# Kernel tuning notes

Measured on AMD Instinct MI355X. Metric: run time of the kernel, lower is better.

## Reference

```python
import jax, jax.numpy as jnp
import numpy as np

N = 200_000          # total nodes
C = 256              # in_channels
B = 64               # batch_size (num graphs)
NPG = N // B         # nodes per graph = max_num_nodes = 3125
E = 3_200_000        # edges (avg degree 16)
RATIO = 0.5
MULTIPLIER = 1.0


def setup_inputs() -> dict:
    key = jax.random.key(0)
    k1, k2, k3, k4, k5, k6 = jax.random.split(key, 6)
    x = jax.random.normal(k1, (N, C), dtype=jnp.float32)
    # hk.initializers.TruncatedNormal() ~ truncated normal, stddev 1
    p = jax.random.truncated_normal(k2, -2.0, 2.0, (C,), dtype=jnp.float32)
    # edges constrained within each graph (realistic graph batching)
    g = jax.random.randint(k3, (E,), 0, B, dtype=jnp.int32)
    senders = g * NPG + jax.random.randint(k4, (E,), 0, NPG, dtype=jnp.int32)
    receivers = g * NPG + jax.random.randint(k5, (E,), 0, NPG, dtype=jnp.int32)
    # sorted batch vector: graph id per node
    batch = jnp.arange(N, dtype=jnp.int32) // NPG
    return {"x": x, "p": p, "senders": senders, "receivers": receivers, "batch": batch}


def _segment_softmax(score, batch, num_segments):
    # batch_softmax from haiku-geometric: numerically-stable per-graph softmax
    mx = jax.ops.segment_max(score, batch, num_segments=num_segments)
    e = jnp.exp(score - mx[batch])
    denom = jax.ops.segment_sum(e, batch, num_segments=num_segments)
    return e / denom[batch]


def reference(x, p, senders, receivers, batch):
    batch_size = B
    num_nodes = x.shape[0]
    # per-node score: <x_i, p>, then softmax within each graph
    score = jnp.sum(x * p, axis=-1)                       # [N]
    score = _segment_softmax(score, batch, batch_size)    # [N]

    # select_batch_topk: keep first k nodes (by position) per graph,
    # move the rest to a new batch id == batch_size.
    nodes_per_batch = jax.ops.segment_sum(
        jnp.ones(num_nodes, dtype=jnp.int32), batch, num_segments=batch_size)
    cum_num_nodes = jnp.concatenate(
        [jnp.zeros(1, jnp.int32), jnp.cumsum(nodes_per_batch)[:-1].astype(jnp.int32)])
    # ratio < 1 branch
    k = jnp.ceil(RATIO * nodes_per_batch).astype(jnp.int32)   # [B]
    index_batch = jnp.arange(num_nodes, dtype=jnp.int32) - cum_num_nodes[batch]
    threshold_per_batch = k[batch] - 1
    new_batch = jnp.where(index_batch <= threshold_per_batch,
                          batch, jnp.full(batch.shape, batch_size, dtype=batch.dtype))

    # gate features by score (multiplier == 1 -> no extra scale)
    x_gated = x * score[:, None]

    # stable sort nodes so dropped nodes go to the end
    new_perm = jnp.argsort(new_batch)          # stable
    x_out = x_gated[new_perm]
    new_batch_sorted = new_batch[new_perm]

    # turn edges touching dropped nodes into self-loops (faithful to source,
    # including the sequential where-overwrite of senders then receivers)
    new_batch_idx = jnp.max(batch) + 1
    mask = (new_batch_sorted[senders] == new_batch_idx) | \
           (new_batch_sorted[receivers] == new_batch_idx)
    senders_out = jnp.where(mask, receivers, senders)
    receivers_out = jnp.where(mask, senders_out, receivers)
    return x_out, senders_out, receivers_out, new_batch_sorted
```

## Files before the change

kernel.cpp:

```cpp
#include <hip/hip_runtime.h>
#include <hip/hip_bf16.h>
#include <stdint.h>


#define RATIO 0.5f

typedef float f32x4 __attribute__((ext_vector_type(4)));
typedef int   i32x4 __attribute__((ext_vector_type(4)));

__global__ __launch_bounds__(256) void k1_scores_boundary(
    const float* __restrict__ x, const float* __restrict__ p,
    const int* __restrict__ batch,
    float* __restrict__ s, int* __restrict__ start, int N) {
    int node0 = blockIdx.x * 8 + (threadIdx.x >> 6) * 2;
    int lane = threadIdx.x & 63;
    if (node0 >= N) return;
    int node1 = node0 + 1;
    const f32x4 pv = *reinterpret_cast<const f32x4*>(p + lane * 4);
    const f32x4 a = *reinterpret_cast<const f32x4*>(x + (size_t)node0 * 256 + lane * 4);
    const f32x4 b = *reinterpret_cast<const f32x4*>(x + (size_t)node1 * 256 + lane * 4);
    float acc0 = a.x * pv.x + a.y * pv.y + a.z * pv.z + a.w * pv.w;
    float acc1 = b.x * pv.x + b.y * pv.y + b.z * pv.z + b.w * pv.w;
    #pragma unroll
    for (int off = 32; off; off >>= 1) {
        acc0 += __shfl_down(acc0, off, 64);
        acc1 += __shfl_down(acc1, off, 64);
    }
    if (lane == 0) {
        s[node0] = acc0;
        s[node1] = acc1;
        int b0 = batch[node0];
        if (node0 == 0 || batch[node0 - 1] != b0) start[b0] = node0;
        int b1 = batch[node1];
        if (batch[node0] != b1) start[b1] = node1;
    }
}

__global__ __launch_bounds__(256) void k2_meta_stats(
    const float* __restrict__ s, const int* __restrict__ start, int N, int B,
    int* __restrict__ kk, int* __restrict__ Kb, int* __restrict__ Db,
    int* __restrict__ Ktot, float* __restrict__ mx, float* __restrict__ denom) {
    if (blockIdx.x == (unsigned)B) {
        int g = threadIdx.x;
        if (g >= B) return;
        int st = start[g];
        int en = (g == B - 1) ? N : start[g + 1];
        int cnt = en - st;
        int kv = (int)ceilf(RATIO * (float)cnt);
        int dv = cnt - kv;
        int kp = kv, dp = dv;
        #pragma unroll
        for (int off = 1; off < 64; off <<= 1) {
            int a = __shfl_up(kp, off, 64);
            int b_ = __shfl_up(dp, off, 64);
            if (g >= off) { kp += a; dp += b_; }
        }
        kk[g] = kv;
        Kb[g] = kp - kv;
        Db[g] = dp - dv;
        if (g == B - 1) *Ktot = kp;
        return;
    }
    int g = blockIdx.x;
    int st = start[g];
    int en = (g == B - 1) ? N : start[g + 1];
    __shared__ float red[256];
    float m = -INFINITY;
    for (int i = st + threadIdx.x; i < en; i += 256) m = fmaxf(m, s[i]);
    red[threadIdx.x] = m; __syncthreads();
    for (int o = 128; o; o >>= 1) {
        if (threadIdx.x < o) red[threadIdx.x] = fmaxf(red[threadIdx.x], red[threadIdx.x + o]);
        __syncthreads();
    }
    m = red[0]; __syncthreads();
    float sum = 0.f;
    for (int i = st + threadIdx.x; i < en; i += 256) sum += expf(s[i] - m);
    red[threadIdx.x] = sum; __syncthreads();
    for (int o = 128; o; o >>= 1) {
        if (threadIdx.x < o) red[threadIdx.x] += red[threadIdx.x + o];
        __syncthreads();
    }
    if (threadIdx.x == 0) { mx[g] = m; denom[g] = red[0]; }
}

__global__ __launch_bounds__(256) void k3_scatter(
    const float* __restrict__ x, const float* __restrict__ s,
    const int* __restrict__ batch, const int* __restrict__ start,
    const int* __restrict__ kk, const int* __restrict__ Kb, const int* __restrict__ Db,
    const int* __restrict__ Ktot, const float* __restrict__ mx, const float* __restrict__ denom,
    int N, int B, float* __restrict__ xout, float* __restrict__ nbout) {
    int node0 = blockIdx.x * 8 + (threadIdx.x >> 6) * 2;
    if (node0 >= N) return;
    int node1 = node0 + 1;
    int lane = threadIdx.x & 63;
    int kt = *Ktot;

    int g0 = batch[node0], g1 = batch[node1];
    int idx0 = node0 - start[g0], idx1 = node1 - start[g1];
    int kv0 = kk[g0], kv1 = kk[g1];
    bool kept0 = idx0 < kv0, kept1 = idx1 < kv1;
    int pos0 = kept0 ? (Kb[g0] + idx0) : (kt + Db[g0] + (idx0 - kv0));
    int pos1 = kept1 ? (Kb[g1] + idx1) : (kt + Db[g1] + (idx1 - kv1));
    float sc0 = expf(s[node0] - mx[g0]) / denom[g0];
    float sc1 = expf(s[node1] - mx[g1]) / denom[g1];

    const f32x4 a = *reinterpret_cast<const f32x4*>(x + (size_t)node0 * 256 + lane * 4);
    const f32x4 b = *reinterpret_cast<const f32x4*>(x + (size_t)node1 * 256 + lane * 4);
    f32x4 oa, ob;
    oa.x = a.x * sc0; oa.y = a.y * sc0; oa.z = a.z * sc0; oa.w = a.w * sc0;
    ob.x = b.x * sc1; ob.y = b.y * sc1; ob.z = b.z * sc1; ob.w = b.w * sc1;
    __builtin_nontemporal_store(oa, reinterpret_cast<f32x4*>(xout + (size_t)pos0 * 256 + lane * 4));
    __builtin_nontemporal_store(ob, reinterpret_cast<f32x4*>(xout + (size_t)pos1 * 256 + lane * 4));
    if (lane == 0) {
        __builtin_nontemporal_store((float)(kept0 ? g0 : B), nbout + pos0);
        __builtin_nontemporal_store((float)(kept1 ? g1 : B), nbout + pos1);
    }
}

__global__ __launch_bounds__(256) void k4_edges(
    const int* __restrict__ snd, const int* __restrict__ rcv, int E,
    const int* __restrict__ Ktot,
    float* __restrict__ sout, float* __restrict__ rout) {
    int t = blockIdx.x * blockDim.x + threadIdx.x;
    long base = (long)t * 8;
    if (base >= E) return;
    int kt = *Ktot;
    if (base + 8 <= E) {
        i32x4 s0 = __builtin_nontemporal_load(reinterpret_cast<const i32x4*>(snd + base));
        i32x4 s1 = __builtin_nontemporal_load(reinterpret_cast<const i32x4*>(snd + base + 4));
        i32x4 r0 = __builtin_nontemporal_load(reinterpret_cast<const i32x4*>(rcv + base));
        i32x4 r1 = __builtin_nontemporal_load(reinterpret_cast<const i32x4*>(rcv + base + 4));
        f32x4 so0, so1, ro0, ro1;
        so0.x = (float)(((s0.x >= kt) || (r0.x >= kt)) ? r0.x : s0.x);
        so0.y = (float)(((s0.y >= kt) || (r0.y >= kt)) ? r0.y : s0.y);
        so0.z = (float)(((s0.z >= kt) || (r0.z >= kt)) ? r0.z : s0.z);
        so0.w = (float)(((s0.w >= kt) || (r0.w >= kt)) ? r0.w : s0.w);
        so1.x = (float)(((s1.x >= kt) || (r1.x >= kt)) ? r1.x : s1.x);
        so1.y = (float)(((s1.y >= kt) || (r1.y >= kt)) ? r1.y : s1.y);
        so1.z = (float)(((s1.z >= kt) || (r1.z >= kt)) ? r1.z : s1.z);
        so1.w = (float)(((s1.w >= kt) || (r1.w >= kt)) ? r1.w : s1.w);
        ro0.x = (float)r0.x; ro0.y = (float)r0.y; ro0.z = (float)r0.z; ro0.w = (float)r0.w;
        ro1.x = (float)r1.x; ro1.y = (float)r1.y; ro1.z = (float)r1.z; ro1.w = (float)r1.w;
        __builtin_nontemporal_store(so0, reinterpret_cast<f32x4*>(sout + base));
        __builtin_nontemporal_store(so1, reinterpret_cast<f32x4*>(sout + base + 4));
        __builtin_nontemporal_store(ro0, reinterpret_cast<f32x4*>(rout + base));
        __builtin_nontemporal_store(ro1, reinterpret_cast<f32x4*>(rout + base + 4));
    } else {
        for (long e = base; e < E; ++e) {
            int sv = snd[e], rv = rcv[e];
            bool m = (sv >= kt) || (rv >= kt);
            sout[e] = (float)(m ? rv : sv);
            rout[e] = (float)rv;
        }
    }
}

extern "C" void kernel_launch(void* const* d_in, const int* in_sizes, int n_in,
                              void* d_out, int out_size, void* d_ws, size_t ws_size,
                              hipStream_t stream) {
    const float* x = (const float*)d_in[0];
    const float* p = (const float*)d_in[1];
    const int* senders = (const int*)d_in[2];
    const int* receivers = (const int*)d_in[3];
    const int* batch = (const int*)d_in[4];

    const int C = in_sizes[1];
    const int E = in_sizes[2];
    const int N = in_sizes[4];
    const int B = 64;

    char* ws = (char*)d_ws;
    float* s   = (float*)ws;
    int* start = (int*)(ws + (size_t)N * 4);
    int* kk    = start + B;
    int* Kb    = kk + B;
    int* Db    = Kb + B;
    int* Ktot  = Db + B;
    float* mx    = (float*)(Ktot + 1);
    float* denom = mx + B;

    float* out   = (float*)d_out;
    float* xout  = out;
    float* sout  = out + (size_t)N * C;
    float* rout  = sout + E;
    float* nbout = rout + E;

    k1_scores_boundary<<<(N + 7) / 8, 256, 0, stream>>>(x, p, batch, s, start, N);
    k2_meta_stats     <<<B + 1, 256, 0, stream>>>(s, start, N, B, kk, Kb, Db, Ktot, mx, denom);
    k3_scatter        <<<(N + 7) / 8, 256, 0, stream>>>(x, s, batch, start, kk, Kb, Db, Ktot,
                                                        mx, denom, N, B, xout, nbout);
    k4_edges          <<<((E + 7) / 8 + 255) / 256, 256, 0, stream>>>(senders, receivers, E,
                                                                      Ktot, sout, rout);
}
```

Measured before the change: 114.8 us.

## Fuse four kernels into one cooperative persistent kernel with grid syncs

```diff
diff --git a/kernel.cpp b/kernel.cpp
--- a/kernel.cpp
+++ b/kernel.cpp
@@ -1,6 +1,9 @@
 #include <hip/hip_runtime.h>
 #include <hip/hip_bf16.h>
+#include <hip/hip_cooperative_groups.h>
 #include <stdint.h>
+
+namespace cg = cooperative_groups;
 
 
 #define RATIO 0.5f
@@ -8,41 +11,70 @@
 typedef float f32x4 __attribute__((ext_vector_type(4)));
 typedef int   i32x4 __attribute__((ext_vector_type(4)));
 
-__global__ __launch_bounds__(256) void k1_scores_boundary(
+__global__ __launch_bounds__(256) void mega(
     const float* __restrict__ x, const float* __restrict__ p,
+    const int* __restrict__ snd, const int* __restrict__ rcv,
     const int* __restrict__ batch,
-    float* __restrict__ s, int* __restrict__ start, int N) {
-    int node0 = blockIdx.x * 8 + (threadIdx.x >> 6) * 2;
-    int lane = threadIdx.x & 63;
-    if (node0 >= N) return;
-    int node1 = node0 + 1;
-    const f32x4 pv = *reinterpret_cast<const f32x4*>(p + lane * 4);
-    const f32x4 a = *reinterpret_cast<const f32x4*>(x + (size_t)node0 * 256 + lane * 4);
-    const f32x4 b = *reinterpret_cast<const f32x4*>(x + (size_t)node1 * 256 + lane * 4);
-    float acc0 = a.x * pv.x + a.y * pv.y + a.z * pv.z + a.w * pv.w;
-    float acc1 = b.x * pv.x + b.y * pv.y + b.z * pv.z + b.w * pv.w;
-    #pragma unroll
-    for (int off = 32; off; off >>= 1) {
-        acc0 += __shfl_down(acc0, off, 64);
-        acc1 += __shfl_down(acc1, off, 64);
+    float* __restrict__ s, int* __restrict__ start,
+    int* __restrict__ kk, int* __restrict__ Kb, int* __restrict__ Db,
+    int* __restrict__ Ktot, float* __restrict__ mx, float* __restrict__ denom,
+    float* __restrict__ xout, float* __restrict__ nbout,
+    float* __restrict__ sout, float* __restrict__ rout,
+    int N, int B, int E) {
+    cg::grid_group grid = cg::this_grid();
+    const int lane = threadIdx.x & 63;
+    const int wid = blockIdx.x * (blockDim.x >> 6) + (threadIdx.x >> 6);
+    const int nwaves = gridDim.x * (blockDim.x >> 6);
+    const int npairs = N >> 1;
+
+    {
+        const f32x4 pv = *reinterpret_cast<const f32x4*>(p + lane * 4);
+        for (int pr = wid; pr < npairs; pr += nwaves) {
+            int node0 = pr * 2, node1 = node0 + 1;
+            const f32x4 a = *reinterpret_cast<const f32x4*>(x + (size_t)node0 * 256 + lane * 4);
+            const f32x4 b = *reinterpret_cast<const f32x4*>(x + (size_t)node1 * 256 + lane * 4);
+            float acc0 = a.x * pv.x + a.y * pv.y + a.z * pv.z + a.w * pv.w;
+            float acc1 = b.x * pv.x + b.y * pv.y + b.z * pv.z + b.w * pv.w;
+            #pragma unroll
+            for (int off = 32; off; off >>= 1) {
+                acc0 += __shfl_down(acc0, off, 64);
+                acc1 += __shfl_down(acc1, off, 64);
+            }
+            if (lane == 0) {
+                s[node0] = acc0;
+                s[node1] = acc1;
+                int b0 = batch[node0];
+                if (node0 == 0 || batch[node0 - 1] != b0) start[b0] = node0;
+                int b1 = batch[node1];
+                if (b0 != b1) start[b1] = node1;
+            }
+        }
     }
-    if (lane == 0) {
-        s[node0] = acc0;
-        s[node1] = acc1;
-        int b0 = batch[node0];
-        if (node0 == 0 || batch[node0 - 1] != b0) start[b0] = node0;
-        int b1 = batch[node1];
-        if (batch[node0] != b1) start[b1] = node1;
-    }
-}
+    grid.sync();
 
-__global__ __launch_bounds__(256) void k2_meta_stats(
-    const float* __restrict__ s, const int* __restrict__ start, int N, int B,
-    int* __restrict__ kk, int* __restrict__ Kb, int* __restrict__ Db,
-    int* __restrict__ Ktot, float* __restrict__ mx, float* __restrict__ denom) {
-    if (blockIdx.x == (unsigned)B) {
+    if (blockIdx.x < (unsigned)B) {
+        int g = blockIdx.x;
+        int st = start[g];
+        int en = (g == B - 1) ? N : start[g + 1];
+        __shared__ float red[256];
+        float m = -INFINITY;
+        for (int i = st + threadIdx.x; i < en; i += 256) m = fmaxf(m, s[i]);
+        red[threadIdx.x] = m; __syncthreads();
+        for (int o = 128; o; o >>= 1) {
+            if (threadIdx.x < o) red[threadIdx.x] = fmaxf(red[threadIdx.x], red[threadIdx.x + o]);
+            __syncthreads();
+        }
+        m = red[0]; __syncthreads();
+        float sum = 0.f;
+        for (int i = st + threadIdx.x; i < en; i += 256) sum += expf(s[i] - m);
+        red[threadIdx.x] = sum; __syncthreads();
+        for (int o = 128; o; o >>= 1) {
+            if (threadIdx.x < o) red[threadIdx.x] += red[threadIdx.x + o];
+            __syncthreads();
+        }
+        if (threadIdx.x == 0) { mx[g] = m; denom[g] = red[0]; }
+    } else if (blockIdx.x == (unsigned)B && threadIdx.x < 64) {
         int g = threadIdx.x;
-        if (g >= B) return;
         int st = start[g];
         int en = (g == B - 1) ? N : start[g + 1];
         int cnt = en - st;
@@ -59,98 +91,66 @@
         Kb[g] = kp - kv;
         Db[g] = dp - dv;
         if (g == B - 1) *Ktot = kp;
-        return;
     }
-    int g = blockIdx.x;
-    int st = start[g];
-    int en = (g == B - 1) ? N : start[g + 1];
-    __shared__ float red[256];
-    float m = -INFINITY;
-    for (int i = st + threadIdx.x; i < en; i += 256) m = fmaxf(m, s[i]);
-    red[threadIdx.x] = m; __syncthreads();
-    for (int o = 128; o; o >>= 1) {
-        if (threadIdx.x < o) red[threadIdx.x] = fmaxf(red[threadIdx.x], red[threadIdx.x + o]);
-        __syncthreads();
+    grid.sync();
+
+    const int kt = *Ktot;
+    for (int pr = wid; pr < npairs; pr += nwaves) {
+        int node0 = pr * 2, node1 = node0 + 1;
+        int g0 = batch[node0], g1 = batch[node1];
+        int idx0 = node0 - start[g0], idx1 = node1 - start[g1];
+        int kv0 = kk[g0], kv1 = kk[g1];
+        bool kept0 = idx0 < kv0, kept1 = idx1 < kv1;
+        int pos0 = kept0 ? (Kb[g0] + idx0) : (kt + Db[g0] + (idx0 - kv0));
+        int pos1 = kept1 ? (Kb[g1] + idx1) : (kt + Db[g1] + (idx1 - kv1));
+        float sc0 = expf(s[node0] - mx[g0]) / denom[g0];
+        float sc1 = expf(s[node1] - mx[g1]) / denom[g1];
+        const f32x4 a = *reinterpret_cast<const f32x4*>(x + (size_t)node0 * 256 + lane * 4);
+        const f32x4 b = *reinterpret_cast<const f32x4*>(x + (size_t)node1 * 256 + lane * 4);
+        f32x4 oa, ob;
+        oa.x = a.x * sc0; oa.y = a.y * sc0; oa.z = a.z * sc0; oa.w = a.w * sc0;
+        ob.x = b.x * sc1; ob.y = b.y * sc1; ob.z = b.z * sc1; ob.w = b.w * sc1;
+        __builtin_nontemporal_store(oa, reinterpret_cast<f32x4*>(xout + (size_t)pos0 * 256 + lane * 4));
+        __builtin_nontemporal_store(ob, reinterpret_cast<f32x4*>(xout + (size_t)pos1 * 256 + lane * 4));
+        if (lane == 0) {
+            __builtin_nontemporal_store((float)(kept0 ? g0 : B), nbout + pos0);
+            __builtin_nontemporal_store((float)(kept1 ? g1 : B), nbout + pos1);
+        }
     }
-    m = red[0]; __syncthreads();
-    float sum = 0.f;
-    for (int i = st + threadIdx.x; i < en; i += 256) sum += expf(s[i] - m);
-    red[threadIdx.x] = sum; __syncthreads();
-    for (int o = 128; o; o >>= 1) {
-        if (threadIdx.x < o) red[threadIdx.x] += red[threadIdx.x + o];
-        __syncthreads();
-    }
-    if (threadIdx.x == 0) { mx[g] = m; denom[g] = red[0]; }
-}
-
-__global__ __launch_bounds__(256) void k3_scatter(
-    const float* __restrict__ x, const float* __restrict__ s,
-    const int* __restrict__ batch, const int* __restrict__ start,
-    const int* __restrict__ kk, const int* __restrict__ Kb, const int* __restrict__ Db,
-    const int* __restrict__ Ktot, const float* __restrict__ mx, const float* __restrict__ denom,
-    int N, int B, float* __restrict__ xout, float* __restrict__ nbout) {
-    int node0 = blockIdx.x * 8 + (threadIdx.x >> 6) * 2;
-    if (node0 >= N) return;
-    int node1 = node0 + 1;
-    int lane = threadIdx.x & 63;
-    int kt = *Ktot;
-
-    int g0 = batch[node0], g1 = batch[node1];
-    int idx0 = node0 - start[g0], idx1 = node1 - start[g1];
-    int kv0 = kk[g0], kv1 = kk[g1];
-    bool kept0 = idx0 < kv0, kept1 = idx1 < kv1;
-    int pos0 = kept0 ? (Kb[g0] + idx0) : (kt + Db[g0] + (idx0 - kv0));
-    int pos1 = kept1 ? (Kb[g1] + idx1) : (kt + Db[g1] + (idx1 - kv1));
-    float sc0 = expf(s[node0] - mx[g0]) / denom[g0];
-    float sc1 = expf(s[node1] - mx[g1]) / denom[g1];
-
-    const f32x4 a = *reinterpret_cast<const f32x4*>(x + (size_t)node0 * 256 + lane * 4);
-    const f32x4 b = *reinterpret_cast<const f32x4*>(x + (size_t)node1 * 256 + lane * 4);
-    f32x4 oa, ob;
-    oa.x = a.x * sc0; oa.y = a.y * sc0; oa.z = a.z * sc0; oa.w = a.w * sc0;
-    ob.x = b.x * sc1; ob.y = b.y * sc1; ob.z = b.z * sc1; ob.w = b.w * sc1;
-    __builtin_nontemporal_store(oa, reinterpret_cast<f32x4*>(xout + (size_t)pos0 * 256 + lane * 4));
-    __builtin_nontemporal_store(ob, reinterpret_cast<f32x4*>(xout + (size_t)pos1 * 256 + lane * 4));
-    if (lane == 0) {
-        __builtin_nontemporal_store((float)(kept0 ? g0 : B), nbout + pos0);
-        __builtin_nontemporal_store((float)(kept1 ? g1 : B), nbout + pos1);
-    }
-}
-
-__global__ __launch_bounds__(256) void k4_edges(
-    const int* __restrict__ snd, const int* __restrict__ rcv, int E,
-    const int* __restrict__ Ktot,
-    float* __restrict__ sout, float* __restrict__ rout) {
-    int t = blockIdx.x * blockDim.x + threadIdx.x;
-    long base = (long)t * 8;
-    if (base >= E) return;
-    int kt = *Ktot;
-    if (base + 8 <= E) {
-        i32x4 s0 = __builtin_nontemporal_load(reinterpret_cast<const i32x4*>(snd + base));
-        i32x4 s1 = __builtin_nontemporal_load(reinterpret_cast<const i32x4*>(snd + base + 4));
-        i32x4 r0 = __builtin_nontemporal_load(reinterpret_cast<const i32x4*>(rcv + base));
-        i32x4 r1 = __builtin_nontemporal_load(reinterpret_cast<const i32x4*>(rcv + base + 4));
-        f32x4 so0, so1, ro0, ro1;
-        so0.x = (float)(((s0.x >= kt) || (r0.x >= kt)) ? r0.x : s0.x);
-        so0.y = (float)(((s0.y >= kt) || (r0.y >= kt)) ? r0.y : s0.y);
-        so0.z = (float)(((s0.z >= kt) || (r0.z >= kt)) ? r0.z : s0.z);
-        so0.w = (float)(((s0.w >= kt) || (r0.w >= kt)) ? r0.w : s0.w);
-        so1.x = (float)(((s1.x >= kt) || (r1.x >= kt)) ? r1.x : s1.x);
-        so1.y = (float)(((s1.y >= kt) || (r1.y >= kt)) ? r1.y : s1.y);
-        so1.z = (float)(((s1.z >= kt) || (r1.z >= kt)) ? r1.z : s1.z);
-        so1.w = (float)(((s1.w >= kt) || (r1.w >= kt)) ? r1.w : s1.w);
-        ro0.x = (float)r0.x; ro0.y = (float)r0.y; ro0.z = (float)r0.z; ro0.w = (float)r0.w;
-        ro1.x = (float)r1.x; ro1.y = (float)r1.y; ro1.z = (float)r1.z; ro1.w = (float)r1.w;
-        __builtin_nontemporal_store(so0, reinterpret_cast<f32x4*>(sout + base));
-        __builtin_nontemporal_store(so1, reinterpret_cast<f32x4*>(sout + base + 4));
-        __builtin_nontemporal_store(ro0, reinterpret_cast<f32x4*>(rout + base));
-        __builtin_nontemporal_store(ro1, reinterpret_cast<f32x4*>(rout + base + 4));
-    } else {
-        for (long e = base; e < E; ++e) {
-            int sv = snd[e], rv = rcv[e];
-            bool m = (sv >= kt) || (rv >= kt);
-            sout[e] = (float)(m ? rv : sv);
-            rout[e] = (float)rv;
+    {
+        int tid = blockIdx.x * blockDim.x + threadIdx.x;
+        int nthr = gridDim.x * blockDim.x;
+        int nchunks = (E + 7) / 8;
+        for (int c = tid; c < nchunks; c += nthr) {
+            long base = (long)c * 8;
+            if (base + 8 <= E) {
+                i32x4 s0 = __builtin_nontemporal_load(reinterpret_cast<const i32x4*>(snd + base));
+                i32x4 s1 = __builtin_nontemporal_load(reinterpret_cast<const i32x4*>(snd + base + 4));
+                i32x4 r0 = __builtin_nontemporal_load(reinterpret_cast<const i32x4*>(rcv + base));
+                i32x4 r1 = __builtin_nontemporal_load(reinterpret_cast<const i32x4*>(rcv + base + 4));
+                f32x4 so0, so1, ro0, ro1;
+                so0.x = (float)(((s0.x >= kt) || (r0.x >= kt)) ? r0.x : s0.x);
+                so0.y = (float)(((s0.y >= kt) || (r0.y >= kt)) ? r0.y : s0.y);
+                so0.z = (float)(((s0.z >= kt) || (r0.z >= kt)) ? r0.z : s0.z);
+                so0.w = (float)(((s0.w >= kt) || (r0.w >= kt)) ? r0.w : s0.w);
+                so1.x = (float)(((s1.x >= kt) || (r1.x >= kt)) ? r1.x : s1.x);
+                so1.y = (float)(((s1.y >= kt) || (r1.y >= kt)) ? r1.y : s1.y);
+                so1.z = (float)(((s1.z >= kt) || (r1.z >= kt)) ? r1.z : s1.z);
+                so1.w = (float)(((s1.w >= kt) || (r1.w >= kt)) ? r1.w : s1.w);
+                ro0.x = (float)r0.x; ro0.y = (float)r0.y; ro0.z = (float)r0.z; ro0.w = (float)r0.w;
+                ro1.x = (float)r1.x; ro1.y = (float)r1.y; ro1.z = (float)r1.z; ro1.w = (float)r1.w;
+                __builtin_nontemporal_store(so0, reinterpret_cast<f32x4*>(sout + base));
+                __builtin_nontemporal_store(so1, reinterpret_cast<f32x4*>(sout + base + 4));
+                __builtin_nontemporal_store(ro0, reinterpret_cast<f32x4*>(rout + base));
+                __builtin_nontemporal_store(ro1, reinterpret_cast<f32x4*>(rout + base + 4));
+            } else {
+                for (long e = base; e < E; ++e) {
+                    int sv = snd[e], rv = rcv[e];
+                    bool m = (sv >= kt) || (rv >= kt);
+                    sout[e] = (float)(m ? rv : sv);
+                    rout[e] = (float)rv;
+                }
+            }
         }
     }
 }
@@ -165,9 +165,9 @@
     const int* batch = (const int*)d_in[4];
 
     const int C = in_sizes[1];
-    const int E = in_sizes[2];
-    const int N = in_sizes[4];
-    const int B = 64;
+    int E = in_sizes[2];
+    int N = in_sizes[4];
+    int B = 64;
 
     char* ws = (char*)d_ws;
     float* s   = (float*)ws;
@@ -185,10 +185,13 @@
     float* rout  = sout + E;
     float* nbout = rout + E;
 
-    k1_scores_boundary<<<(N + 7) / 8, 256, 0, stream>>>(x, p, batch, s, start, N);
-    k2_meta_stats     <<<B + 1, 256, 0, stream>>>(s, start, N, B, kk, Kb, Db, Ktot, mx, denom);
-    k3_scatter        <<<(N + 7) / 8, 256, 0, stream>>>(x, s, batch, start, kk, Kb, Db, Ktot,
-                                                        mx, denom, N, B, xout, nbout);
-    k4_edges          <<<((E + 7) / 8 + 255) / 256, 256, 0, stream>>>(senders, receivers, E,
-                                                                      Ktot, sout, rout);
+    void* args[] = {
+        (void*)&x, (void*)&p, (void*)&senders, (void*)&receivers, (void*)&batch,
+        (void*)&s, (void*)&start, (void*)&kk, (void*)&Kb, (void*)&Db,
+        (void*)&Ktot, (void*)&mx, (void*)&denom,
+        (void*)&xout, (void*)&nbout, (void*)&sout, (void*)&rout,
+        (void*)&N, (void*)&B, (void*)&E
+    };
+    hipLaunchCooperativeKernel((const void*)mega, dim3(1024), dim3(256),
+                               args, 0, stream);
 }
```

Result: slower. 323.8 us (+182.0%).
